# Kernel optimization log

Hardware: AMD Instinct MI355X
Metric: run time of the kernel (lower is better)

## Reference

```python
import jax, jax.numpy as jnp
import numpy as np

B, S, D, H = 2, 2048, 1024, 16
DK = D // H  # 64
SCALE = DK ** (-0.5)  # NOTE: module divides by this, i.e. multiplies scores by sqrt(DK)


def setup_inputs() -> dict:
    key = jax.random.key(0)
    ks = jax.random.split(key, 9)
    std = D ** (-0.5)
    return {
        "x": jax.random.normal(ks[0], (B, S, D), dtype=jnp.float32),
        "attention_mask": jnp.ones((B, S), dtype=jnp.int32),
        "Wq": jax.random.normal(ks[1], (D, D), dtype=jnp.float32) * std,
        "bq": jnp.zeros((D,), dtype=jnp.float32),
        "Wk": jax.random.normal(ks[2], (D, D), dtype=jnp.float32) * std,
        "bk": jnp.zeros((D,), dtype=jnp.float32),
        "Wv": jax.random.normal(ks[3], (D, D), dtype=jnp.float32) * std,
        "bv": jnp.zeros((D,), dtype=jnp.float32),
        "Wo": jax.random.normal(ks[4], (D, D), dtype=jnp.float32) * std,
        "bo": jnp.zeros((D,), dtype=jnp.float32),
    }


def _split_heads(t):
    # [B, S, D] -> [B, H, S, DK]
    return t.reshape(B, S, H, DK).transpose(0, 2, 1, 3)


def reference(x, attention_mask, Wq, bq, Wk, bk, Wv, bv, Wo, bo):
    q = _split_heads(x @ Wq.T + bq)
    k = _split_heads(x @ Wk.T + bk)
    v = _split_heads(x @ Wv.T + bv)

    # faithful to source: sim = (q @ k^T) / scale with scale = dk**-0.5
    sim = jnp.einsum("bhqd,bhkd->bhqk", q, k) / SCALE

    # key-padding mask: positions where attention_mask == 0 are masked out
    neg = jnp.finfo(sim.dtype).min
    keep = attention_mask.astype(bool)[:, None, None, :]  # [B,1,1,S]
    sim = jnp.where(keep, sim, neg)

    attn = jax.nn.softmax(sim, axis=-1)  # dropout is identity at inference
    out = jnp.einsum("bhqk,bhkd->bhqd", attn, v)
    out = out.transpose(0, 2, 1, 3).reshape(B, S, D)  # merge heads
    return out @ Wo.T + bo
```

## Files before the change

kernel.cpp:

```cpp
#include <hip/hip_runtime.h>
#include <hip/hip_bf16.h>
#include <math.h>

#define BB 2
#define SS 2048
#define DD 1024
#define HH 16
#define DKK 64
#define BH (BB * HH)

typedef __bf16 bf16_t;
typedef _Float16 f16_t;
typedef __attribute__((ext_vector_type(8))) _Float16 f16x8;
typedef __attribute__((ext_vector_type(4))) _Float16 f16x4;
typedef __attribute__((ext_vector_type(4))) float f32x4;
typedef __attribute__((ext_vector_type(4))) int i32x4;
typedef __attribute__((ext_vector_type(2))) int i32x2;

#define GLD_LDS(gp, lp) __builtin_amdgcn_global_load_lds( \
    (const __attribute__((address_space(1))) void*)(gp),  \
    (__attribute__((address_space(3))) void*)(lp), 16, 0, 0)

static __device__ __forceinline__ int pkrtz(float a, float b) {
    auto h = __builtin_amdgcn_cvt_pkrtz(a, b);
    return __builtin_bit_cast(int, h);
}

__global__ void cast_x_flags(const float* __restrict__ in, f16_t* __restrict__ out,
                             const int* __restrict__ mask, int* __restrict__ flags, int n) {
    int i = blockIdx.x * blockDim.x + threadIdx.x;
    int stride = gridDim.x * blockDim.x;
    for (; i < n; i += stride) out[i] = (f16_t)in[i];
    if (blockIdx.x == 0 && threadIdx.x < BB * (SS / 128)) {
        int f = threadIdx.x;
        int b = f / (SS / 128), t = f % (SS / 128);
        const int* p = mask + b * SS + t * 128;
        int all = 1;
        for (int j = 0; j < 128; ++j) all &= (p[j] != 0);
        flags[f] = all;
    }
}

__global__ void cast_wqk(const float* __restrict__ Wq, const float* __restrict__ Wk,
                         f16_t* __restrict__ hi, f16_t* __restrict__ lo, int nw) {
    int i = blockIdx.x * blockDim.x + threadIdx.x;
    int stride = gridDim.x * blockDim.x;
    for (; i < 2 * nw; i += stride) {
        float v = (i < nw) ? Wq[i] : Wk[i - nw];
        f16_t h = (f16_t)v;
        hi[i] = h;
        lo[i] = (f16_t)(v - (float)h);
    }
}

__global__ void cast_wvo(const float* __restrict__ Wv, const float* __restrict__ Wo,
                         f16_t* __restrict__ wv, f16_t* __restrict__ wo, int nw) {
    int i = blockIdx.x * blockDim.x + threadIdx.x;
    int stride = gridDim.x * blockDim.x;
    for (; i < 2 * nw; i += stride) {
        if (i < nw) wv[i] = (f16_t)Wv[i];
        else        wo[i - nw] = (f16_t)Wo[i - nw];
    }
}

__global__ __launch_bounds__(256) void gemm_qkv(const f16_t* __restrict__ Af,
                                                const f16_t* __restrict__ Wqkh,
                                                const f16_t* __restrict__ Wqkl,
                                                const f16_t* __restrict__ Wvf,
                                                const float* __restrict__ bq,
                                                const float* __restrict__ bk,
                                                const float* __restrict__ bv,
                                                f16_t* __restrict__ q_o,
                                                f16_t* __restrict__ k_o,
                                                f16_t* __restrict__ vt_o,
                                                int K) {
    __shared__ __align__(16) f16_t sA[4096];
    __shared__ __align__(16) f16_t sB0[4096];
    __shared__ __align__(16) f16_t sB1[4096];

    const int tid  = threadIdx.x;
    const int wv   = tid >> 6;
    const int lane = tid & 63;
    const int quad = lane >> 4;
    const int l15  = lane & 15;
    const int wr   = wv >> 1;
    const int wc   = wv & 1;
    const int row0 = blockIdx.y * 128;
    const int col0 = blockIdx.x * 128;
    const bool isV = (col0 >= 2048);

    const f16_t* B0 = isV ? (Wvf + (long)(col0 - 2048) * K) : (Wqkh + (long)col0 * K);
    const f16_t* B1 = isV ? nullptr : (Wqkl + (long)col0 * K);

    f32x4 acc[4][4] = {};

    const int srow = tid >> 2;
    const int scol = (tid & 3) * 8;
    const long aoff = (long)(row0 + srow) * K + scol;
    const long boff = (long)srow * K + scol;

    if (isV) {
#pragma unroll 1
        for (int kb = 0; kb < K; kb += 32) {
#pragma unroll
            for (int p = 0; p < 2; ++p) {
                const long go = (long)p * 64 * K + kb;
                const int lo = p * 2048 + wv * 512;
                GLD_LDS(Af + aoff + go, sA + lo);
                GLD_LDS(B0 + boff + go, sB0 + lo);
            }
            __syncthreads();
            f16x8 af[4];
#pragma unroll
            for (int mt = 0; mt < 4; ++mt)
                af[mt] = *(const f16x8*)&sA[(wr * 64 + mt * 16 + l15) * 32 + quad * 8];
#pragma unroll
            for (int nt = 0; nt < 4; ++nt) {
                f16x8 b0 = *(const f16x8*)&sB0[(wc * 64 + nt * 16 + l15) * 32 + quad * 8];
#pragma unroll
                for (int mt = 0; mt < 4; ++mt)
                    acc[mt][nt] = __builtin_amdgcn_mfma_f32_16x16x32_f16(af[mt], b0, acc[mt][nt], 0, 0, 0);
            }
            __syncthreads();
        }
    } else {
#pragma unroll 1
        for (int kb = 0; kb < K; kb += 32) {
#pragma unroll
            for (int p = 0; p < 2; ++p) {
                const long go = (long)p * 64 * K + kb;
                const int lo = p * 2048 + wv * 512;
                GLD_LDS(Af + aoff + go, sA + lo);
                GLD_LDS(B0 + boff + go, sB0 + lo);
                GLD_LDS(B1 + boff + go, sB1 + lo);
            }
            __syncthreads();
            f16x8 af[4];
#pragma unroll
            for (int mt = 0; mt < 4; ++mt)
                af[mt] = *(const f16x8*)&sA[(wr * 64 + mt * 16 + l15) * 32 + quad * 8];
#pragma unroll
            for (int nt = 0; nt < 4; ++nt) {
                f16x8 b0 = *(const f16x8*)&sB0[(wc * 64 + nt * 16 + l15) * 32 + quad * 8];
                f16x8 b1 = *(const f16x8*)&sB1[(wc * 64 + nt * 16 + l15) * 32 + quad * 8];
#pragma unroll
                for (int mt = 0; mt < 4; ++mt) {
                    acc[mt][nt] = __builtin_amdgcn_mfma_f32_16x16x32_f16(af[mt], b0, acc[mt][nt], 0, 0, 0);
                    acc[mt][nt] = __builtin_amdgcn_mfma_f32_16x16x32_f16(af[mt], b1, acc[mt][nt], 0, 0, 0);
                }
            }
            __syncthreads();
        }
    }

    if (isV) {
#pragma unroll
        for (int nt = 0; nt < 4; ++nt) {
            const int colv = (col0 - 2048) + wc * 64 + nt * 16 + l15;
            const float bvv = bv[colv];
            const int hq = colv >> 6, dk = colv & 63;
#pragma unroll
            for (int mt = 0; mt < 4; ++mt) {
                const int grow0 = row0 + wr * 64 + mt * 16 + quad * 4;
                const int bq2 = grow0 >> 11;
                const int s0  = grow0 & (SS - 1);
                f16x4 pk;
#pragma unroll
                for (int r = 0; r < 4; ++r) pk[r] = (f16_t)(acc[mt][nt][r] + bvv);
                *(f16x4*)(vt_o + ((long)(bq2 * HH + hq) * DKK + dk) * SS + s0) = pk;
            }
        }
    } else {
        const bool isK = (col0 >= 1024);
        const float* bias = isK ? bk : bq;
        f16_t* op = isK ? k_o : q_o;
#pragma unroll
        for (int nt = 0; nt < 4; ++nt) {
            const int gcol = (col0 & 1023) + wc * 64 + nt * 16 + l15;
            const float bvv = bias[gcol];
            const int hq = gcol >> 6, dk = gcol & 63;
#pragma unroll
            for (int mt = 0; mt < 4; ++mt) {
                const int grow0 = row0 + wr * 64 + mt * 16 + quad * 4;
#pragma unroll
                for (int r = 0; r < 4; ++r) {
                    int grow = grow0 + r;
                    float vvv = acc[mt][nt][r] + bvv;
                    long off = (((long)(grow >> 11) * HH + hq) * SS + (grow & (SS - 1))) * DKK + dk;
                    op[off] = (f16_t)vvv;
                }
            }
        }
    }
}

__global__ __launch_bounds__(256) void gemm_o(const f16_t* __restrict__ Ah,
                                              const f16_t* __restrict__ Bhp,
                                              const float* __restrict__ bias,
                                              float* __restrict__ outf,
                                              int N, int K) {
    __shared__ __align__(16) f16_t lds[2048 + 4096];
    f16_t* Ash = lds;
    f16_t* Bsh = lds + 2048;

    const int tid  = threadIdx.x;
    const int wv   = tid >> 6;
    const int lane = tid & 63;
    const int quad = lane >> 4;
    const int l15  = lane & 15;
    const int wr   = wv >> 1;
    const int wc   = wv & 1;
    const int row0 = blockIdx.y * 64;
    const int col0 = blockIdx.x * 128;

    f32x4 acc[2][4] = {};

    const int srow = lane >> 2;
    const int scol = (lane & 3) * 8;
    const f16_t* gA  = Ah  + (long)(row0 + wv * 16 + srow) * K + scol;
    const f16_t* gB0 = Bhp + (long)(col0 + wv * 16 + srow) * K + scol;
    const f16_t* gB1 = Bhp + (long)(col0 + (wv + 4) * 16 + srow) * K + scol;
    f16_t* lA  = Ash + wv * 512;
    f16_t* lB0 = Bsh + wv * 512;
    f16_t* lB1 = Bsh + (wv + 4) * 512;

#pragma unroll 1
    for (int kb = 0; kb < K; kb += 32) {
        GLD_LDS(gA + kb, lA);
        GLD_LDS(gB0 + kb, lB0);
        GLD_LDS(gB1 + kb, lB1);
        __syncthreads();

        f16x8 af[2];
#pragma unroll
        for (int mt = 0; mt < 2; ++mt)
            af[mt] = *(const f16x8*)&Ash[(wr * 32 + mt * 16 + l15) * 32 + quad * 8];
#pragma unroll
        for (int nt = 0; nt < 4; ++nt) {
            f16x8 bh = *(const f16x8*)&Bsh[(wc * 64 + nt * 16 + l15) * 32 + quad * 8];
#pragma unroll
            for (int mt = 0; mt < 2; ++mt)
                acc[mt][nt] = __builtin_amdgcn_mfma_f32_16x16x32_f16(af[mt], bh, acc[mt][nt], 0, 0, 0);
        }
        __syncthreads();
    }

#pragma unroll
    for (int mt = 0; mt < 2; ++mt) {
#pragma unroll
        for (int nt = 0; nt < 4; ++nt) {
            const int gcol  = col0 + wc * 64 + nt * 16 + l15;
            const float bvv = bias[gcol];
            const int grow0 = row0 + wr * 32 + mt * 16 + quad * 4;
#pragma unroll
            for (int r = 0; r < 4; ++r)
                outf[(long)(grow0 + r) * N + gcol] = acc[mt][nt][r] + bvv;
        }
    }
}

__global__ __launch_bounds__(256) void attn_mfma8(const f16_t* __restrict__ Qp,
                                                  const f16_t* __restrict__ Kp,
                                                  const f16_t* __restrict__ Vtp,
                                                  const int* __restrict__ mask,
                                                  const int* __restrict__ flags,
                                                  f16_t* __restrict__ ctx,
                                                  int seq_len) {
    __shared__ __align__(16) f16_t Ksh[2][2][4096];
    __shared__ __align__(16) f16_t Vsh[2][2][4096];

    const int tid  = threadIdx.x;
    const int wv   = tid >> 6;
    const int lane = tid & 63;
    const int quad = lane >> 4;
    const int l15  = lane & 15;
    const int bh   = blockIdx.y;
    const int b    = bh >> 4;
    const int h    = bh & 15;
    const int q0   = blockIdx.x * 64 + wv * 16;

    const long kb = (long)bh * SS * DKK;

    f16x8 qf[2];
    {
        const f16_t* pq = Qp + kb + (long)(q0 + l15) * DKK + quad * 8;
        qf[0] = *(const f16x8*)pq;
        qf[1] = *(const f16x8*)(pq + 32);
        const f16_t qs = (f16_t)(8.0f * 1.44269504088896f);
#pragma unroll
        for (int j = 0; j < 8; ++j) { qf[0][j] *= qs; qf[1][j] *= qs; }
    }

    f16x4 ones4;
#pragma unroll
    for (int j = 0; j < 4; ++j) ones4[j] = (f16_t)1.0f;

    f32x4 o[4], lacc;
#pragma unroll
    for (int r = 0; r < 4; ++r) o[r] = (f32x4){0.f, 0.f, 0.f, 0.f};
    lacc = (f32x4){0.f, 0.f, 0.f, 0.f};
    float m = -1e30f;

    const int* mrow = mask + b * SS;
    const int* frow = flags + b * (SS / 128);

    const int srow8 = lane >> 3;
    const int gcolB = ((lane & 7) ^ srow8) * 8;
    const int NT = seq_len >> 7;

#pragma unroll
    for (int c = 0; c < 2; ++c) {
#pragma unroll
        for (int p = 0; p < 2; ++p) {
            const int i = wv * 2 + p;
            const int row = i * 8 + srow8;
            GLD_LDS(Kp + kb + (long)(c * 64 + row) * DKK + gcolB, &Ksh[0][c][i * 512]);
            GLD_LDS(Vtp + kb + (long)row * SS + c * 64 + gcolB, &Vsh[0][c][i * 512]);
        }
    }

#pragma unroll 1
    for (int tt = 0; tt < NT; ++tt) {
        const int cur = tt & 1;
        const int kt = tt << 7;
        __syncthreads();

        if (tt + 1 < NT) {
            const int kn = (tt + 1) << 7;
#pragma unroll
            for (int c = 0; c < 2; ++c) {
#pragma unroll
                for (int p = 0; p < 2; ++p) {
                    const int i = wv * 2 + p;
                    const int row = i * 8 + srow8;
                    GLD_LDS(Kp + kb + (long)(kn + c * 64 + row) * DKK + gcolB, &Ksh[cur ^ 1][c][i * 512]);
                    GLD_LDS(Vtp + kb + (long)row * SS + kn + c * 64 + gcolB, &Vsh[cur ^ 1][c][i * 512]);
                }
            }
        }

        f32x4 s[8];
#pragma unroll
        for (int nt = 0; nt < 8; ++nt) s[nt] = (f32x4){0.f, 0.f, 0.f, 0.f};
#pragma unroll
        for (int nt = 0; nt < 8; ++nt) {
            const int c = nt >> 2;
            const int kr = (nt & 3) * 16 + l15;
#pragma unroll
            for (int dt = 0; dt < 2; ++dt) {
                f16x8 kf = *(const f16x8*)&Ksh[cur][c][kr * 64 + (((dt * 4 + quad) ^ (l15 & 7)) << 3)];
                s[nt] = __builtin_amdgcn_mfma_f32_16x16x32_f16(kf, qf[dt], s[nt], 0, 0, 0);
            }
        }

        if (!frow[kt >> 7]) {
#pragma unroll
            for (int nt = 0; nt < 8; ++nt) {
                i32x4 kp = *(const i32x4*)&mrow[kt + nt * 16 + quad * 4];
#pragma unroll
                for (int r = 0; r < 4; ++r)
                    s[nt][r] = kp[r] ? s[nt][r] : -1e30f;
            }
        }

        f32x4 mx;
#pragma unroll
        for (int r = 0; r < 4; ++r)
            mx[r] = fmaxf(fmaxf(fmaxf(s[0][r], s[1][r]), fmaxf(s[2][r], s[3][r])),
                          fmaxf(fmaxf(s[4][r], s[5][r]), fmaxf(s[6][r], s[7][r])));
        float tm = fmaxf(fmaxf(mx[0], mx[1]), fmaxf(mx[2], mx[3]));
        tm = fmaxf(tm, __shfl_xor(tm, 16));
        tm = fmaxf(tm, __shfl_xor(tm, 32));

        const float mn = fmaxf(m, tm);
        if (__any(tm > m)) {
            const float alpha = exp2f(m - mn);
            float a4[4];
#pragma unroll
            for (int r = 0; r < 4; ++r)
                a4[r] = __shfl(alpha, quad * 4 + r);
#pragma unroll
            for (int t = 0; t < 4; ++t)
#pragma unroll
                for (int r = 0; r < 4; ++r) o[t][r] *= a4[r];
#pragma unroll
            for (int r = 0; r < 4; ++r) lacc[r] *= a4[r];
        }
        m = mn;

#pragma unroll
        for (int nt = 0; nt < 8; ++nt) {
            const int c = nt >> 2;
            float p0 = exp2f(s[nt][0] - mn);
            float p1 = exp2f(s[nt][1] - mn);
            float p2 = exp2f(s[nt][2] - mn);
            float p3 = exp2f(s[nt][3] - mn);
            i32x2 pp;
            pp[0] = pkrtz(p0, p1);
            pp[1] = pkrtz(p2, p3);
            f16x4 paf = __builtin_bit_cast(f16x4, pp);
            lacc = __builtin_amdgcn_mfma_f32_16x16x16f16(paf, ones4, lacc, 0, 0, 0);
            const int vcol = ((((nt & 3) * 2 + (quad >> 1)) ^ (l15 & 7)) << 3) + ((quad & 1) << 2);
#pragma unroll
            for (int t = 0; t < 4; ++t) {
                f16x4 vB = *(const f16x4*)&Vsh[cur][c][(t * 16 + l15) * 64 + vcol];
                o[t] = __builtin_amdgcn_mfma_f32_16x16x16f16(paf, vB, o[t], 0, 0, 0);
            }
        }
    }

    float inv[4];
#pragma unroll
    for (int r = 0; r < 4; ++r) inv[r] = 1.0f / lacc[r];
#pragma unroll
    for (int t = 0; t < 4; ++t) {
        int d = t * 16 + l15;
#pragma unroll
        for (int r = 0; r < 4; ++r) {
            int tok = b * SS + q0 + quad * 4 + r;
            ctx[(long)tok * DD + h * DKK + d] = (f16_t)(o[t][r] * inv[r]);
        }
    }
}

extern "C" void kernel_launch(void* const* d_in, const int* in_sizes, int n_in,
                              void* d_out, int out_size, void* d_ws, size_t ws_size,
                              hipStream_t stream) {
    const float* x  = (const float*)d_in[0];
    const int* mask = (const int*)d_in[1];
    const float* Wq = (const float*)d_in[2];
    const float* bq = (const float*)d_in[3];
    const float* Wk = (const float*)d_in[4];
    const float* bk = (const float*)d_in[5];
    const float* Wv = (const float*)d_in[6];
    const float* bv = (const float*)d_in[7];
    const float* Wo = (const float*)d_in[8];
    const float* bo = (const float*)d_in[9];
    float* out = (float*)d_out;

    const long NX = (long)BB * SS * DD;
    const long NW = (long)DD * DD;

    char* ws = (char*)d_ws;
    f16_t* xf   = (f16_t*)ws; ws += NX * 2;
    f16_t* wqkh = (f16_t*)ws; ws += 2 * NW * 2;
    f16_t* wqkl = (f16_t*)ws; ws += 2 * NW * 2;
    f16_t* wvf  = (f16_t*)ws; ws += NW * 2;
    f16_t* wof  = (f16_t*)ws; ws += NW * 2;
    f16_t* qf   = (f16_t*)ws; ws += NX * 2;
    f16_t* kf   = (f16_t*)ws; ws += NX * 2;
    f16_t* vt   = (f16_t*)ws; ws += NX * 2;
    f16_t* ctx  = (f16_t*)ws; ws += NX * 2;
    int*   flg  = (int*)ws;   ws += 64 * 4;

    cast_x_flags<<<2048, 256, 0, stream>>>(x, xf, mask, flg, (int)NX);
    cast_wqk<<<2048, 256, 0, stream>>>(Wq, Wk, wqkh, wqkl, (int)NW);
    cast_wvo<<<2048, 256, 0, stream>>>(Wv, Wo, wvf, wof, (int)NW);

    dim3 gqkv(3 * DD / 128, (BB * SS) / 128);
    gemm_qkv<<<gqkv, 256, 0, stream>>>(xf, wqkh, wqkl, wvf, bq, bk, bv, qf, kf, vt, DD);

    dim3 agrid(SS / 64, BH);
    attn_mfma8<<<agrid, 256, 0, stream>>>(qf, kf, vt, mask, flg, ctx, SS);

    dim3 go(DD / 128, (BB * SS) / 64);
    gemm_o<<<go, 256, 0, stream>>>(ctx, wof, bo, out, DD, DD);
}
```

Measured before the change: 288.1 us.

## Process two query tiles per wave in attention to reuse K/V shared-memory fragments

Each wave now handles two 16-row query tiles, 64 rows apart, instead of one, so every block covers 128 queries and the grid halves. Each K and V fragment read from shared memory feeds two MFMAs, which halves LDS traffic and global K/V loads per query. The cost is roughly double the accumulator and score registers, which may lower occupancy, and there are half as many blocks (512) to spread across the CUs.

After: 273.7 us. 1.05x faster.

```diff
diff --git a/kernel.cpp b/kernel.cpp
--- a/kernel.cpp
+++ b/kernel.cpp
@@ -259,7 +259,7 @@
     }
 }
 
-__global__ __launch_bounds__(256) void attn_mfma8(const f16_t* __restrict__ Qp,
+__global__ __launch_bounds__(256) void attn_mfma9(const f16_t* __restrict__ Qp,
                                                   const f16_t* __restrict__ Kp,
                                                   const f16_t* __restrict__ Vtp,
                                                   const int* __restrict__ mask,
@@ -277,29 +277,39 @@
     const int bh   = blockIdx.y;
     const int b    = bh >> 4;
     const int h    = bh & 15;
-    const int q0   = blockIdx.x * 64 + wv * 16;
+    const int q0   = blockIdx.x * 128 + wv * 16;
 
     const long kb = (long)bh * SS * DKK;
 
-    f16x8 qf[2];
+    f16x8 qf0[2], qf1[2];
     {
         const f16_t* pq = Qp + kb + (long)(q0 + l15) * DKK + quad * 8;
-        qf[0] = *(const f16x8*)pq;
-        qf[1] = *(const f16x8*)(pq + 32);
+        qf0[0] = *(const f16x8*)pq;
+        qf0[1] = *(const f16x8*)(pq + 32);
+        const f16_t* pq1 = pq + 64 * DKK;
+        qf1[0] = *(const f16x8*)pq1;
+        qf1[1] = *(const f16x8*)(pq1 + 32);
         const f16_t qs = (f16_t)(8.0f * 1.44269504088896f);
 #pragma unroll
-        for (int j = 0; j < 8; ++j) { qf[0][j] *= qs; qf[1][j] *= qs; }
+        for (int j = 0; j < 8; ++j) {
+            qf0[0][j] *= qs; qf0[1][j] *= qs;
+            qf1[0][j] *= qs; qf1[1][j] *= qs;
+        }
     }
 
     f16x4 ones4;
 #pragma unroll
     for (int j = 0; j < 4; ++j) ones4[j] = (f16_t)1.0f;
 
-    f32x4 o[4], lacc;
-#pragma unroll
-    for (int r = 0; r < 4; ++r) o[r] = (f32x4){0.f, 0.f, 0.f, 0.f};
-    lacc = (f32x4){0.f, 0.f, 0.f, 0.f};
-    float m = -1e30f;
+    f32x4 o0[4], o1[4], lacc0, lacc1;
+#pragma unroll
+    for (int r = 0; r < 4; ++r) {
+        o0[r] = (f32x4){0.f, 0.f, 0.f, 0.f};
+        o1[r] = (f32x4){0.f, 0.f, 0.f, 0.f};
+    }
+    lacc0 = (f32x4){0.f, 0.f, 0.f, 0.f};
+    lacc1 = (f32x4){0.f, 0.f, 0.f, 0.f};
+    float m0 = -1e30f, m1 = -1e30f;
 
     const int* mrow = mask + b * SS;
     const int* frow = flags + b * (SS / 128);
@@ -339,9 +349,12 @@
             }
         }
 
-        f32x4 s[8];
-#pragma unroll
-        for (int nt = 0; nt < 8; ++nt) s[nt] = (f32x4){0.f, 0.f, 0.f, 0.f};
+        f32x4 s0[8], s1[8];
+#pragma unroll
+        for (int nt = 0; nt < 8; ++nt) {
+            s0[nt] = (f32x4){0.f, 0.f, 0.f, 0.f};
+            s1[nt] = (f32x4){0.f, 0.f, 0.f, 0.f};
+        }
 #pragma unroll
         for (int nt = 0; nt < 8; ++nt) {
             const int c = nt >> 2;
@@ -349,7 +362,8 @@
 #pragma unroll
             for (int dt = 0; dt < 2; ++dt) {
                 f16x8 kf = *(const f16x8*)&Ksh[cur][c][kr * 64 + (((dt * 4 + quad) ^ (l15 & 7)) << 3)];
-                s[nt] = __builtin_amdgcn_mfma_f32_16x16x32_f16(kf, qf[dt], s[nt], 0, 0, 0);
+                s0[nt] = __builtin_amdgcn_mfma_f32_16x16x32_f16(kf, qf0[dt], s0[nt], 0, 0, 0);
+                s1[nt] = __builtin_amdgcn_mfma_f32_16x16x32_f16(kf, qf1[dt], s1[nt], 0, 0, 0);
             }
         }
 
@@ -358,67 +372,93 @@
             for (int nt = 0; nt < 8; ++nt) {
                 i32x4 kp = *(const i32x4*)&mrow[kt + nt * 16 + quad * 4];
 #pragma unroll
-                for (int r = 0; r < 4; ++r)
-                    s[nt][r] = kp[r] ? s[nt][r] : -1e30f;
-            }
-        }
-
-        f32x4 mx;
-#pragma unroll
-        for (int r = 0; r < 4; ++r)
-            mx[r] = fmaxf(fmaxf(fmaxf(s[0][r], s[1][r]), fmaxf(s[2][r], s[3][r])),
-                          fmaxf(fmaxf(s[4][r], s[5][r]), fmaxf(s[6][r], s[7][r])));
-        float tm = fmaxf(fmaxf(mx[0], mx[1]), fmaxf(mx[2], mx[3]));
-        tm = fmaxf(tm, __shfl_xor(tm, 16));
-        tm = fmaxf(tm, __shfl_xor(tm, 32));
-
-        const float mn = fmaxf(m, tm);
-        if (__any(tm > m)) {
-            const float alpha = exp2f(m - mn);
+                for (int r = 0; r < 4; ++r) {
+                    s0[nt][r] = kp[r] ? s0[nt][r] : -1e30f;
+                    s1[nt][r] = kp[r] ? s1[nt][r] : -1e30f;
+                }
+            }
+        }
+
+        f32x4 mxa, mxb;
+#pragma unroll
+        for (int r = 0; r < 4; ++r) {
+            mxa[r] = fmaxf(fmaxf(fmaxf(s0[0][r], s0[1][r]), fmaxf(s0[2][r], s0[3][r])),
+                           fmaxf(fmaxf(s0[4][r], s0[5][r]), fmaxf(s0[6][r], s0[7][r])));
+            mxb[r] = fmaxf(fmaxf(fmaxf(s1[0][r], s1[1][r]), fmaxf(s1[2][r], s1[3][r])),
+                           fmaxf(fmaxf(s1[4][r], s1[5][r]), fmaxf(s1[6][r], s1[7][r])));
+        }
+        float tm0 = fmaxf(fmaxf(mxa[0], mxa[1]), fmaxf(mxa[2], mxa[3]));
+        float tm1 = fmaxf(fmaxf(mxb[0], mxb[1]), fmaxf(mxb[2], mxb[3]));
+        tm0 = fmaxf(tm0, __shfl_xor(tm0, 16));
+        tm1 = fmaxf(tm1, __shfl_xor(tm1, 16));
+        tm0 = fmaxf(tm0, __shfl_xor(tm0, 32));
+        tm1 = fmaxf(tm1, __shfl_xor(tm1, 32));
+
+        const float mn0 = fmaxf(m0, tm0);
+        const float mn1 = fmaxf(m1, tm1);
+        if (__any(tm0 > m0)) {
+            const float alpha = exp2f(m0 - mn0);
             float a4[4];
 #pragma unroll
-            for (int r = 0; r < 4; ++r)
-                a4[r] = __shfl(alpha, quad * 4 + r);
+            for (int r = 0; r < 4; ++r) a4[r] = __shfl(alpha, quad * 4 + r);
 #pragma unroll
             for (int t = 0; t < 4; ++t)
 #pragma unroll
-                for (int r = 0; r < 4; ++r) o[t][r] *= a4[r];
-#pragma unroll
-            for (int r = 0; r < 4; ++r) lacc[r] *= a4[r];
-        }
-        m = mn;
+                for (int r = 0; r < 4; ++r) o0[t][r] *= a4[r];
+#pragma unroll
+            for (int r = 0; r < 4; ++r) lacc0[r] *= a4[r];
+        }
+        if (__any(tm1 > m1)) {
+            const float alpha = exp2f(m1 - mn1);
+            float a4[4];
+#pragma unroll
+            for (int r = 0; r < 4; ++r) a4[r] = __shfl(alpha, quad * 4 + r);
+#pragma unroll
+            for (int t = 0; t < 4; ++t)
+#pragma unroll
+                for (int r = 0; r < 4; ++r) o1[t][r] *= a4[r];
+#pragma unroll
+            for (int r = 0; r < 4; ++r) lacc1[r] *= a4[r];
+        }
+        m0 = mn0;
+        m1 = mn1;
 
 #pragma unroll
         for (int nt = 0; nt < 8; ++nt) {
             const int c = nt >> 2;
-            float p0 = exp2f(s[nt][0] - mn);
-            float p1 = exp2f(s[nt][1] - mn);
-            float p2 = exp2f(s[nt][2] - mn);
-            float p3 = exp2f(s[nt][3] - mn);
-            i32x2 pp;
-            pp[0] = pkrtz(p0, p1);
-            pp[1] = pkrtz(p2, p3);
-            f16x4 paf = __builtin_bit_cast(f16x4, pp);
-            lacc = __builtin_amdgcn_mfma_f32_16x16x16f16(paf, ones4, lacc, 0, 0, 0);
+            i32x2 pp0, pp1;
+            pp0[0] = pkrtz(exp2f(s0[nt][0] - mn0), exp2f(s0[nt][1] - mn0));
+            pp0[1] = pkrtz(exp2f(s0[nt][2] - mn0), exp2f(s0[nt][3] - mn0));
+            pp1[0] = pkrtz(exp2f(s1[nt][0] - mn1), exp2f(s1[nt][1] - mn1));
+            pp1[1] = pkrtz(exp2f(s1[nt][2] - mn1), exp2f(s1[nt][3] - mn1));
+            f16x4 paf0 = __builtin_bit_cast(f16x4, pp0);
+            f16x4 paf1 = __builtin_bit_cast(f16x4, pp1);
+            lacc0 = __builtin_amdgcn_mfma_f32_16x16x16f16(paf0, ones4, lacc0, 0, 0, 0);
+            lacc1 = __builtin_amdgcn_mfma_f32_16x16x16f16(paf1, ones4, lacc1, 0, 0, 0);
             const int vcol = ((((nt & 3) * 2 + (quad >> 1)) ^ (l15 & 7)) << 3) + ((quad & 1) << 2);
 #pragma unroll
             for (int t = 0; t < 4; ++t) {
                 f16x4 vB = *(const f16x4*)&Vsh[cur][c][(t * 16 + l15) * 64 + vcol];
-                o[t] = __builtin_amdgcn_mfma_f32_16x16x16f16(paf, vB, o[t], 0, 0, 0);
-            }
-        }
-    }
-
-    float inv[4];
-#pragma unroll
-    for (int r = 0; r < 4; ++r) inv[r] = 1.0f / lacc[r];
+                o0[t] = __builtin_amdgcn_mfma_f32_16x16x16f16(paf0, vB, o0[t], 0, 0, 0);
+                o1[t] = __builtin_amdgcn_mfma_f32_16x16x16f16(paf1, vB, o1[t], 0, 0, 0);
+            }
+        }
+    }
+
+    float inv0[4], inv1[4];
+#pragma unroll
+    for (int r = 0; r < 4; ++r) {
+        inv0[r] = 1.0f / lacc0[r];
+        inv1[r] = 1.0f / lacc1[r];
+    }
 #pragma unroll
     for (int t = 0; t < 4; ++t) {
         int d = t * 16 + l15;
 #pragma unroll
         for (int r = 0; r < 4; ++r) {
             int tok = b * SS + q0 + quad * 4 + r;
-            ctx[(long)tok * DD + h * DKK + d] = (f16_t)(o[t][r] * inv[r]);
+            ctx[(long)tok * DD + h * DKK + d] = (f16_t)(o0[t][r] * inv0[r]);
+            ctx[(long)(tok + 64) * DD + h * DKK + d] = (f16_t)(o1[t][r] * inv1[r]);
         }
     }
 }
@@ -460,8 +500,8 @@
     dim3 gqkv(3 * DD / 128, (BB * SS) / 128);
     gemm_qkv<<<gqkv, 256, 0, stream>>>(xf, wqkh, wqkl, wvf, bq, bk, bv, qf, kf, vt, DD);
 
-    dim3 agrid(SS / 64, BH);
-    attn_mfma8<<<agrid, 256, 0, stream>>>(qf, kf, vt, mask, flg, ctx, SS);
+    dim3 agrid(SS / 128, BH);
+    attn_mfma9<<<agrid, 256, 0, stream>>>(qf, kf, vt, mask, flg, ctx, SS);
 
     dim3 go(DD / 128, (BB * SS) / 64);
     gemm_o<<<go, 256, 0, stream>>>(ctx, wof, bo, out, DD, DD);
```

## Fuse prep casts into one kernel and widen attention blocks to 8 waves

Applied to the files above, without the earlier changes.

Merges the three input-cast kernels into a single launch to cut launch overhead. The attention kernel now uses 512 threads covering 128 queries per block, so each staged K/V tile is shared by twice as many waves. K is held in a single buffer that is refilled after the QK MFMAs behind an extra barrier, while V stays double-buffered. This lowers LDS use per query and doubles K/V reuse, at the cost of an extra __syncthreads per tile and less overlap of the K load with compute.

Measured after the change: 262.9 us. -8.8%, faster.

```diff
diff --git a/kernel.cpp b/kernel.cpp
--- a/kernel.cpp
+++ b/kernel.cpp
@@ -26,40 +26,40 @@
     return __builtin_bit_cast(int, h);
 }
 
-__global__ void cast_x_flags(const float* __restrict__ in, f16_t* __restrict__ out,
-                             const int* __restrict__ mask, int* __restrict__ flags, int n) {
+__global__ void prep_all(const float* __restrict__ x, const int* __restrict__ mask,
+                         const float* __restrict__ Wq, const float* __restrict__ Wk,
+                         const float* __restrict__ Wv, const float* __restrict__ Wo,
+                         f16_t* __restrict__ xf,
+                         f16_t* __restrict__ wqkh, f16_t* __restrict__ wqkl,
+                         f16_t* __restrict__ wvf, f16_t* __restrict__ wof,
+                         int* __restrict__ flags) {
+    const int NXi = BB * SS * DD;
+    const int NWi = DD * DD;
+    const int total = NXi + 4 * NWi;
     int i = blockIdx.x * blockDim.x + threadIdx.x;
-    int stride = gridDim.x * blockDim.x;
-    for (; i < n; i += stride) out[i] = (f16_t)in[i];
+    const int stride = gridDim.x * blockDim.x;
+    for (; i < total; i += stride) {
+        if (i < NXi) {
+            xf[i] = (f16_t)x[i];
+        } else if (i < NXi + 2 * NWi) {
+            const int j = i - NXi;
+            const float v = (j < NWi) ? Wq[j] : Wk[j - NWi];
+            const f16_t h = (f16_t)v;
+            wqkh[j] = h;
+            wqkl[j] = (f16_t)(v - (float)h);
+        } else {
+            const int j = i - NXi - 2 * NWi;
+            if (j < NWi) wvf[j] = (f16_t)Wv[j];
+            else         wof[j - NWi] = (f16_t)Wo[j - NWi];
+        }
+    }
     if (blockIdx.x == 0 && threadIdx.x < BB * (SS / 128)) {
-        int f = threadIdx.x;
-        int b = f / (SS / 128), t = f % (SS / 128);
+        const int f = threadIdx.x;
+        const int b = f / (SS / 128), t = f % (SS / 128);
         const int* p = mask + b * SS + t * 128;
         int all = 1;
         for (int j = 0; j < 128; ++j) all &= (p[j] != 0);
         flags[f] = all;
-    }
-}
-
-__global__ void cast_wqk(const float* __restrict__ Wq, const float* __restrict__ Wk,
-                         f16_t* __restrict__ hi, f16_t* __restrict__ lo, int nw) {
-    int i = blockIdx.x * blockDim.x + threadIdx.x;
-    int stride = gridDim.x * blockDim.x;
-    for (; i < 2 * nw; i += stride) {
-        float v = (i < nw) ? Wq[i] : Wk[i - nw];
-        f16_t h = (f16_t)v;
-        hi[i] = h;
-        lo[i] = (f16_t)(v - (float)h);
-    }
-}
-
-__global__ void cast_wvo(const float* __restrict__ Wv, const float* __restrict__ Wo,
-                         f16_t* __restrict__ wv, f16_t* __restrict__ wo, int nw) {
-    int i = blockIdx.x * blockDim.x + threadIdx.x;
-    int stride = gridDim.x * blockDim.x;
-    for (; i < 2 * nw; i += stride) {
-        if (i < nw) wv[i] = (f16_t)Wv[i];
-        else        wo[i - nw] = (f16_t)Wo[i - nw];
     }
 }
 
@@ -259,14 +259,14 @@
     }
 }
 
-__global__ __launch_bounds__(256) void attn_mfma8(const f16_t* __restrict__ Qp,
-                                                  const f16_t* __restrict__ Kp,
-                                                  const f16_t* __restrict__ Vtp,
-                                                  const int* __restrict__ mask,
-                                                  const int* __restrict__ flags,
-                                                  f16_t* __restrict__ ctx,
-                                                  int seq_len) {
-    __shared__ __align__(16) f16_t Ksh[2][2][4096];
+__global__ __launch_bounds__(512, 4) void attn_mfma12(const f16_t* __restrict__ Qp,
+                                                      const f16_t* __restrict__ Kp,
+                                                      const f16_t* __restrict__ Vtp,
+                                                      const int* __restrict__ mask,
+                                                      const int* __restrict__ flags,
+                                                      f16_t* __restrict__ ctx,
+                                                      int seq_len) {
+    __shared__ __align__(16) f16_t Ksh[2][4096];
     __shared__ __align__(16) f16_t Vsh[2][2][4096];
 
     const int tid  = threadIdx.x;
@@ -277,7 +277,7 @@
     const int bh   = blockIdx.y;
     const int b    = bh >> 4;
     const int h    = bh & 15;
-    const int q0   = blockIdx.x * 64 + wv * 16;
+    const int q0   = blockIdx.x * 128 + wv * 16;
 
     const long kb = (long)bh * SS * DKK;
 
@@ -310,13 +310,9 @@
 
 #pragma unroll
     for (int c = 0; c < 2; ++c) {
-#pragma unroll
-        for (int p = 0; p < 2; ++p) {
-            const int i = wv * 2 + p;
-            const int row = i * 8 + srow8;
-            GLD_LDS(Kp + kb + (long)(c * 64 + row) * DKK + gcolB, &Ksh[0][c][i * 512]);
-            GLD_LDS(Vtp + kb + (long)row * SS + c * 64 + gcolB, &Vsh[0][c][i * 512]);
-        }
+        const int row = wv * 8 + srow8;
+        GLD_LDS(Kp + kb + (long)(c * 64 + row) * DKK + gcolB, &Ksh[c][wv * 512]);
+        GLD_LDS(Vtp + kb + (long)row * SS + c * 64 + gcolB, &Vsh[0][c][wv * 512]);
     }
 
 #pragma unroll 1
@@ -325,20 +321,6 @@
         const int kt = tt << 7;
         __syncthreads();
 
-        if (tt + 1 < NT) {
-            const int kn = (tt + 1) << 7;
-#pragma unroll
-            for (int c = 0; c < 2; ++c) {
-#pragma unroll
-                for (int p = 0; p < 2; ++p) {
-                    const int i = wv * 2 + p;
-                    const int row = i * 8 + srow8;
-                    GLD_LDS(Kp + kb + (long)(kn + c * 64 + row) * DKK + gcolB, &Ksh[cur ^ 1][c][i * 512]);
-                    GLD_LDS(Vtp + kb + (long)row * SS + kn + c * 64 + gcolB, &Vsh[cur ^ 1][c][i * 512]);
-                }
-            }
-        }
-
         f32x4 s[8];
 #pragma unroll
         for (int nt = 0; nt < 8; ++nt) s[nt] = (f32x4){0.f, 0.f, 0.f, 0.f};
@@ -348,8 +330,19 @@
             const int kr = (nt & 3) * 16 + l15;
 #pragma unroll
             for (int dt = 0; dt < 2; ++dt) {
-                f16x8 kf = *(const f16x8*)&Ksh[cur][c][kr * 64 + (((dt * 4 + quad) ^ (l15 & 7)) << 3)];
+                f16x8 kf = *(const f16x8*)&Ksh[c][kr * 64 + (((dt * 4 + quad) ^ (l15 & 7)) << 3)];
                 s[nt] = __builtin_amdgcn_mfma_f32_16x16x32_f16(kf, qf[dt], s[nt], 0, 0, 0);
+            }
+        }
+
+        __syncthreads();
+        if (tt + 1 < NT) {
+            const int kn = (tt + 1) << 7;
+#pragma unroll
+            for (int c = 0; c < 2; ++c) {
+                const int row = wv * 8 + srow8;
+                GLD_LDS(Kp + kb + (long)(kn + c * 64 + row) * DKK + gcolB, &Ksh[c][wv * 512]);
+                GLD_LDS(Vtp + kb + (long)row * SS + kn + c * 64 + gcolB, &Vsh[cur ^ 1][c][wv * 512]);
             }
         }
 
@@ -377,8 +370,7 @@
             const float alpha = exp2f(m - mn);
             float a4[4];
 #pragma unroll
-            for (int r = 0; r < 4; ++r)
-                a4[r] = __shfl(alpha, quad * 4 + r);
+            for (int r = 0; r < 4; ++r) a4[r] = __shfl(alpha, quad * 4 + r);
 #pragma unroll
             for (int t = 0; t < 4; ++t)
 #pragma unroll
@@ -391,13 +383,9 @@
 #pragma unroll
         for (int nt = 0; nt < 8; ++nt) {
             const int c = nt >> 2;
-            float p0 = exp2f(s[nt][0] - mn);
-            float p1 = exp2f(s[nt][1] - mn);
-            float p2 = exp2f(s[nt][2] - mn);
-            float p3 = exp2f(s[nt][3] - mn);
             i32x2 pp;
-            pp[0] = pkrtz(p0, p1);
-            pp[1] = pkrtz(p2, p3);
+            pp[0] = pkrtz(exp2f(s[nt][0] - mn), exp2f(s[nt][1] - mn));
+            pp[1] = pkrtz(exp2f(s[nt][2] - mn), exp2f(s[nt][3] - mn));
             f16x4 paf = __builtin_bit_cast(f16x4, pp);
             lacc = __builtin_amdgcn_mfma_f32_16x16x16f16(paf, ones4, lacc, 0, 0, 0);
             const int vcol = ((((nt & 3) * 2 + (quad >> 1)) ^ (l15 & 7)) << 3) + ((quad & 1) << 2);
@@ -453,15 +441,14 @@
     f16_t* ctx  = (f16_t*)ws; ws += NX * 2;
     int*   flg  = (int*)ws;   ws += 64 * 4;
 
-    cast_x_flags<<<2048, 256, 0, stream>>>(x, xf, mask, flg, (int)NX);
-    cast_wqk<<<2048, 256, 0, stream>>>(Wq, Wk, wqkh, wqkl, (int)NW);
-    cast_wvo<<<2048, 256, 0, stream>>>(Wv, Wo, wvf, wof, (int)NW);
+    prep_all<<<2048, 256, 0, stream>>>(x, mask, Wq, Wk, Wv, Wo,
+                                       xf, wqkh, wqkl, wvf, wof, flg);
 
     dim3 gqkv(3 * DD / 128, (BB * SS) / 128);
     gemm_qkv<<<gqkv, 256, 0, stream>>>(xf, wqkh, wqkl, wvf, bq, bk, bv, qf, kf, vt, DD);
 
-    dim3 agrid(SS / 64, BH);
-    attn_mfma8<<<agrid, 256, 0, stream>>>(qf, kf, vt, mask, flg, ctx, SS);
+    dim3 agrid(SS / 128, BH);
+    attn_mfma12<<<agrid, 512, 0, stream>>>(qf, kf, vt, mask, flg, ctx, SS);
 
     dim3 go(DD / 128, (BB * SS) / 64);
     gemm_o<<<go, 256, 0, stream>>>(ctx, wof, bo, out, DD, DD);
```
